# Performance work log

Hardware: AMD Instinct MI355X
Metric: run time of the kernel (lower is better)

Reference implementation:

```python
import jax, jax.numpy as jnp
import numpy as np

C = 512
CTX = 768
HEADS = 8
GROUPS = min(8, C)
EPS = 1e-5


def setup_inputs() -> dict:
    key = jax.random.key(0)
    ks = jax.random.split(key, 10)
    B, H, W, S = 16, 32, 32, 77
    s_in = 1.0 / np.sqrt(C)
    s_ctx = 1.0 / np.sqrt(CTX)
    return {
        "x": jax.random.normal(ks[0], (B, C, H, W), jnp.float32),
        "context": jax.random.normal(ks[1], (B, S, CTX), jnp.float32),
        "gn_w": jnp.ones((C,), jnp.float32),
        "gn_b": jnp.zeros((C,), jnp.float32),
        "q_w": jax.random.normal(ks[2], (C, C), jnp.float32) * s_in,
        "q_b": jnp.zeros((C,), jnp.float32),
        "kv_w": jax.random.normal(ks[3], (2 * C, CTX), jnp.float32) * s_ctx,
        "kv_b": jnp.zeros((2 * C,), jnp.float32),
        "proj_w": jax.random.normal(ks[4], (C, C), jnp.float32) * s_in,
        "proj_b": jnp.zeros((C,), jnp.float32),
    }


def _group_norm(x, w, b):
    # x: [B, C, H, W]; normalize per group over (C/G, H, W)
    B, Cc, H, W = x.shape
    xg = x.reshape(B, GROUPS, Cc // GROUPS, H * W)
    mean = xg.mean(axis=(2, 3), keepdims=True)
    var = xg.var(axis=(2, 3), keepdims=True)
    xn = (xg - mean) * jax.lax.rsqrt(var + EPS)
    xn = xn.reshape(B, Cc, H, W)
    return xn * w[None, :, None, None] + b[None, :, None, None]


def reference(x, context, gn_w, gn_b, q_w, q_b, kv_w, kv_b, proj_w, proj_b):
    B, Cc, H, W = x.shape
    hd = Cc // HEADS
    h = _group_norm(x, gn_w, gn_b).reshape(B, Cc, H * W)
    # 1x1 conv Q == channel-mixing GEMM
    q = jnp.einsum("oc,bcn->bon", q_w, h) + q_b[None, :, None]  # [B, C, HW]
    q = q.reshape(B, HEADS, hd, H * W).transpose(0, 1, 3, 2)      # [B, h, HW, d]
    S = context.shape[1]
    kv = jnp.einsum("bsc,oc->bso", context, kv_w) + kv_b           # [B, S, 2C]
    kv = kv.reshape(B, S, 2, HEADS, hd)
    k = kv[:, :, 0].transpose(0, 2, 1, 3)                          # [B, h, S, d]
    v = kv[:, :, 1].transpose(0, 2, 1, 3)
    scale = hd ** (-0.5)
    attn = jax.nn.softmax(jnp.einsum("bhnd,bhsd->bhns", q, k) * scale, axis=-1)
    out = jnp.einsum("bhns,bhsd->bhnd", attn, v)                   # [B, h, HW, d]
    out = out.transpose(0, 1, 3, 2).reshape(B, Cc, H * W)
    out = jnp.einsum("oc,bcn->bon", proj_w, out) + proj_b[None, :, None]
    return x + out.reshape(B, Cc, H, W)
```

## Files before the change

### kernel.cpp

```cpp
#include <hip/hip_runtime.h>

#define B_   16
#define C_   512
#define HW_  1024
#define S_   77
#define CTX_ 768
#define HEADS_ 8
#define G_   8
#define EPS_ 1e-5f

typedef unsigned short u16;
typedef unsigned int u32;
typedef __attribute__((ext_vector_type(8))) short bfx8;
typedef __attribute__((ext_vector_type(4))) float fx4;

union U2 { u16 h[4]; uint2 v; };

__device__ __forceinline__ u16 f2bf(float f) {
  union { float f; u32 u; } v; v.f = f;
  u32 u = v.u;
  return (u16)((u + 0x7FFFu + ((u >> 16) & 1u)) >> 16);
}

__device__ __forceinline__ void gload16(const u16* g, u16* l) {
  __builtin_amdgcn_global_load_lds((const __attribute__((address_space(1))) u32*)g,
                                   (__attribute__((address_space(3))) u32*)l, 16, 0, 0);
}

__device__ __forceinline__ void castw_body(const float* __restrict__ in,
                                           u16* __restrict__ out, int K, int i, int n4) {
  if (i >= n4) return;
  float4 v = *(const float4*)(in + (size_t)i * 4);
  int K4 = K >> 2;
  int m = i / K4;
  int k = (i - m * K4) * 4;
  int pb = ((k & 63) >> 3) ^ (m & 7);
  size_t dst = (size_t)m * K + (k & ~63) + (pb << 3) + (k & 7);
  U2 pk;
  pk.h[0] = f2bf(v.x); pk.h[1] = f2bf(v.y); pk.h[2] = f2bf(v.z); pk.h[3] = f2bf(v.w);
  *(uint2*)(out + dst) = pk.v;
}

__device__ __forceinline__ void castctx_body(const float* __restrict__ in,
                                             u16* __restrict__ out, int i) {
  if (i >= 16 * 77 * 192) return;
  int rg = i / 192;
  int k = (i - rg * 192) * 4;
  int b = rg / 77, s = rg - b * 77;
  float4 v = *(const float4*)(in + (size_t)i * 4);
  int pb = ((k & 63) >> 3) ^ (s & 7);
  size_t dst = ((size_t)b * 128 + s) * 768 + (k & ~63) + (pb << 3) + (k & 7);
  U2 pk;
  pk.h[0] = f2bf(v.x); pk.h[1] = f2bf(v.y); pk.h[2] = f2bf(v.z); pk.h[3] = f2bf(v.w);
  *(uint2*)(out + dst) = pk.v;
}

__device__ __forceinline__ void gnstats_body(const float* __restrict__ x,
                                             float2* __restrict__ part, int blk, int t) {
  int bg = blk >> 3, slice = blk & 7;
  const float4* x4 = (const float4*)(x + (size_t)bg * 65536);
  float s = 0.f, ss = 0.f;
  #pragma unroll
  for (int j = 0; j < 8; ++j) {
    float4 v = x4[slice * 2048 + j * 256 + t];
    s  += v.x + v.y + v.z + v.w;
    ss += v.x*v.x + v.y*v.y + v.z*v.z + v.w*v.w;
  }
  #pragma unroll
  for (int off = 32; off; off >>= 1) {
    s  += __shfl_down(s, off);
    ss += __shfl_down(ss, off);
  }
  __shared__ float rs[4], rss[4];
  int wid = t >> 6;
  if ((t & 63) == 0) { rs[wid] = s; rss[wid] = ss; }
  __syncthreads();
  if (t == 0)
    part[blk] = make_float2(rs[0] + rs[1] + rs[2] + rs[3],
                            rss[0] + rss[1] + rss[2] + rss[3]);
}

__global__ __launch_bounds__(256) void prep_kernel(const float* __restrict__ q_w,
                                                   const float* __restrict__ kv_w,
                                                   const float* __restrict__ proj_w,
                                                   const float* __restrict__ ctx,
                                                   const float* __restrict__ x,
                                                   u16* __restrict__ qw_bf,
                                                   u16* __restrict__ kvw_bf,
                                                   u16* __restrict__ pjw_bf,
                                                   u16* __restrict__ ctx_bf,
                                                   float2* __restrict__ gpart) {
  int bid = blockIdx.x, t = threadIdx.x;
  if (bid < 256)        castw_body(q_w,    qw_bf,  512, bid * 256 + t, 65536);
  else if (bid < 1024)  castw_body(kv_w,   kvw_bf, 768, (bid - 256) * 256 + t, 196608);
  else if (bid < 1280)  castw_body(proj_w, pjw_bf, 512, (bid - 1024) * 256 + t, 65536);
  else if (bid < 2204)  castctx_body(ctx, ctx_bf, (bid - 1280) * 256 + t);
  else                  gnstats_body(x, gpart, bid - 2204, t);
}

__device__ void gn_apply_body(int blk, const float* __restrict__ x,
                              const float* __restrict__ w,
                              const float* __restrict__ bgn,
                              const float2* __restrict__ gpart,
                              u16* __restrict__ hT, u16* __restrict__ T2) {
  int nt = blk & 7, bg = blk >> 3;
  int batch = bg >> 3, g = bg & 7;
  const float4* x4 = (const float4*)(x + ((size_t)batch * C_ + (size_t)g * 64) * HW_);
  float s = 0.f, ss = 0.f;
  #pragma unroll
  for (int j = 0; j < 8; ++j) { float2 pp = gpart[bg * 8 + j]; s += pp.x; ss += pp.y; }
  const float invN = 1.0f / 65536.0f;
  float mean = s * invN;
  float rstd = rsqrtf(ss * invN - mean * mean + EPS_);
  int t = threadIdx.x;
  int n4i = t & 31;
  int c4b = t >> 5;
  #pragma unroll
  for (int j = 0; j < 2; ++j) {
    int c4 = c4b + j * 8;
    float4 v[4];
    float wcs[4], bcs[4];
    #pragma unroll
    for (int e = 0; e < 4; ++e) {
      int c = c4 * 4 + e;
      v[e] = x4[(size_t)c * 256 + nt * 32 + n4i];
      int cg = g * 64 + c;
      float wc_ = w[cg] * rstd;
      wcs[e] = wc_;
      bcs[e] = bgn[cg] - mean * wc_;
    }
    int cbase = c4 * 4;
    #pragma unroll
    for (int ne = 0; ne < 4; ++ne) {
      int n = n4i * 4 + ne;
      int pb = (cbase >> 3) ^ (n & 7);
      U2 pk;
      pk.h[0] = f2bf(((const float*)&v[0])[ne] * wcs[0] + bcs[0]);
      pk.h[1] = f2bf(((const float*)&v[1])[ne] * wcs[1] + bcs[1]);
      pk.h[2] = f2bf(((const float*)&v[2])[ne] * wcs[2] + bcs[2]);
      pk.h[3] = f2bf(((const float*)&v[3])[ne] * wcs[3] + bcs[3]);
      *(uint2*)&T2[n * 72 + (pb << 3) + (cbase & 7)] = pk.v;
    }
  }
  __syncthreads();
  #pragma unroll
  for (int j = 0; j < 4; ++j) {
    int idx = j * 256 + t;
    int row = idx >> 3, cs = (idx & 7) * 8;
    uint4 vv = *(const uint4*)&T2[row * 72 + cs];
    *(uint4*)(hT + ((size_t)batch * 1024 + nt * 128 + row) * 512 + g * 64 + cs) = vv;
  }
}

__device__ void kvgemm_body(int blk, const u16* __restrict__ A, const u16* __restrict__ Bw,
                            const float* __restrict__ bias,
                            u16* __restrict__ o16a, u16* __restrict__ o16b,
                            u16* __restrict__ SH) {
  u16* As = SH;
  u16* Bs = SH + 4096;
  int t = threadIdx.x;
  int b = blk >> 6;
  int m0 = ((blk >> 5) & 1) * 64;
  int n0 = (blk & 31) * 32;
  const u16* aBase = A + (size_t)b * 98304 + (size_t)(m0 + (t >> 3)) * 768 + (t & 7) * 8;
  const u16* bBase = Bw + (size_t)(n0 + (t >> 3)) * 768 + (t & 7) * 8;
  int wid = t >> 6, l = t & 63;
  int wr = wid & 1, wc = wid >> 1;
  int lr = l & 15, lg = l >> 4, xr = lr & 7;
  fx4 acc[2];
  acc[0] = (fx4){0.f, 0.f, 0.f, 0.f};
  acc[1] = (fx4){0.f, 0.f, 0.f, 0.f};

  for (int k0 = 0; k0 < 768; k0 += 64) {
    __syncthreads();
    #pragma unroll
    for (int i = 0; i < 2; ++i)
      gload16(aBase + k0 + (size_t)i * 32 * 768, As + i * 2048 + t * 8);
    gload16(bBase + k0, Bs + t * 8);
    __syncthreads();
    #pragma unroll
    for (int kk = 0; kk < 2; ++kk) {
      int lb = kk * 4 + lg;
      bfx8 bf = *(const bfx8*)&Bs[(wc * 16 + lr) * 64 + ((lb ^ xr) << 3)];
      #pragma unroll
      for (int mi = 0; mi < 2; ++mi) {
        bfx8 af = *(const bfx8*)&As[(wr * 32 + mi * 16 + lr) * 64 + ((lb ^ xr) << 3)];
        acc[mi] = __builtin_amdgcn_mfma_f32_16x16x32_bf16(af, bf, acc[mi], 0, 0, 0);
      }
    }
  }

  int o = n0 + wc * 16 + lr;
  float bb = bias[o];
  #pragma unroll
  for (int mi = 0; mi < 2; ++mi) {
    int sb = m0 + wr * 32 + mi * 16 + lg * 4;
    if (o < 512) {
      #pragma unroll
      for (int r = 0; r < 4; ++r) {
        int sidx = sb + r;
        if (sidx < 96) {
          int ob = (o & ~63) | (((((o >> 3) & 7) ^ (sidx & 7))) << 3) | (o & 7);
          o16a[(size_t)b * 49152 + (size_t)sidx * 512 + ob] = f2bf(acc[mi][r] + bb);
        }
      }
    } else if (sb < 96) {
      U2 pk;
      #pragma unroll
      for (int r = 0; r < 4; ++r)
        pk.h[r] = (sb + r < S_) ? f2bf(acc[mi][r] + bb) : (u16)0;
      *(uint2*)(o16b + (size_t)b * 49152 + (size_t)(o - 512) * 96 + sb) = pk.v;
    }
  }
}

__global__ __launch_bounds__(256) void mid_kernel(const float* __restrict__ x,
                                                  const float* __restrict__ gn_w,
                                                  const float* __restrict__ gn_b,
                                                  const float2* __restrict__ gpart,
                                                  u16* __restrict__ hT,
                                                  const u16* __restrict__ ctx_bf,
                                                  const u16* __restrict__ kvw_bf,
                                                  const float* __restrict__ kv_b,
                                                  u16* __restrict__ kvT_k,
                                                  u16* __restrict__ kvV) {
  __shared__ u16 SH[9216];
  int bid = blockIdx.x;
  if (bid < 1024) gn_apply_body(bid, x, gn_w, gn_b, gpart, hT, SH);
  else            kvgemm_body(bid - 1024, ctx_bf, kvw_bf, kv_b, kvT_k, kvV, SH);
}

__global__ __launch_bounds__(256) void gemm2_kernel(
    const u16* __restrict__ A, const u16* __restrict__ Bw,
    const float* __restrict__ bias, const float* __restrict__ resid,
    float* __restrict__ outf, int K, size_t strideA)
{
  __shared__ u16 As[128 * 64];
  __shared__ u16 Bs[128 * 64];
  int t = threadIdx.x;
  int b = blockIdx.z;
  int n0 = blockIdx.x * 128, m0 = blockIdx.y * 128;
  const u16* aBase = A + (size_t)b * strideA + (size_t)(m0 + (t >> 3)) * K + (t & 7) * 8;
  const u16* bBase = Bw + (size_t)(n0 + (t >> 3)) * K + (t & 7) * 8;
  int wid = t >> 6, l = t & 63;
  int wr = wid >> 1, wc = wid & 1;
  int lr = l & 15, lg = l >> 4;
  fx4 acc[4][4];
  #pragma unroll
  for (int i = 0; i < 4; ++i)
    #pragma unroll
    for (int j = 0; j < 4; ++j) acc[i][j] = (fx4){0.f, 0.f, 0.f, 0.f};

  for (int k0 = 0; k0 < K; k0 += 64) {
    __syncthreads();
    #pragma unroll
    for (int i = 0; i < 4; ++i) {
      gload16(aBase + k0 + (size_t)i * 32 * K, As + i * 2048 + t * 8);
      gload16(bBase + k0 + (size_t)i * 32 * K, Bs + i * 2048 + t * 8);
    }
    __syncthreads();
    #pragma unroll
    for (int kk = 0; kk < 2; ++kk) {
      bfx8 af[4], bf[4];
      int xr = (lr & 7);
      #pragma unroll
      for (int i = 0; i < 4; ++i) {
        int lb = kk * 4 + lg;
        af[i] = *(const bfx8*)&As[(wr * 64 + i * 16 + lr) * 64 + ((lb ^ xr) << 3)];
        bf[i] = *(const bfx8*)&Bs[(wc * 64 + i * 16 + lr) * 64 + ((lb ^ xr) << 3)];
      }
      #pragma unroll
      for (int mi = 0; mi < 4; ++mi)
        #pragma unroll
        for (int ni = 0; ni < 4; ++ni)
          acc[mi][ni] = __builtin_amdgcn_mfma_f32_16x16x32_bf16(af[mi], bf[ni], acc[mi][ni], 0, 0, 0);
    }
  }

  float* O = outf + (size_t)b * 524288;
  const float* R = resid + (size_t)b * 524288;
  #pragma unroll
  for (int ni = 0; ni < 4; ++ni) {
    int cc = n0 + wc * 64 + ni * 16 + lr;
    float bb = bias[cc];
    #pragma unroll
    for (int mi = 0; mi < 4; ++mi) {
      size_t off = (size_t)cc * 1024 + m0 + wr * 64 + mi * 16 + lg * 4;
      float4 rv = *(const float4*)(R + off);
      float4 ov;
      ov.x = acc[mi][ni][0] + bb + rv.x;
      ov.y = acc[mi][ni][1] + bb + rv.y;
      ov.z = acc[mi][ni][2] + bb + rv.z;
      ov.w = acc[mi][ni][3] + bb + rv.w;
      *(float4*)(O + off) = ov;
    }
  }
}

__global__ __launch_bounds__(256) void qattn_kernel(const u16* __restrict__ hT,
                                                    const u16* __restrict__ qw,
                                                    const float* __restrict__ q_b,
                                                    const u16* __restrict__ kvK,
                                                    const u16* __restrict__ kvV,
                                                    u16* __restrict__ aoT) {
  __shared__ u16 SH[12288];
  u16* QO = SH;
  u16* As = SH + 4096;
  u16* Bs = SH + 8192;
  u16* Ps = SH + 4096;

  int t = threadIdx.x;
  int n0 = blockIdx.x * 64, head = blockIdx.y, b = blockIdx.z;
  int wid = t >> 6, l = t & 63;
  int lr = l & 15, lg = l >> 4, xr = lr & 7;
  int qbase = wid * 16;

  {
    const u16* aBase = hT + (size_t)b * 524288 + (size_t)(n0 + (t >> 3)) * 512 + (t & 7) * 8;
    const u16* bBase = qw + (size_t)(head * 64 + (t >> 3)) * 512 + (t & 7) * 8;
    fx4 acc[4];
    #pragma unroll
    for (int j = 0; j < 4; ++j) acc[j] = (fx4){0.f, 0.f, 0.f, 0.f};
    for (int k0 = 0; k0 < 512; k0 += 64) {
      __syncthreads();
      #pragma unroll
      for (int i = 0; i < 2; ++i) {
        gload16(aBase + k0 + (size_t)i * 32 * 512, As + i * 2048 + t * 8);
        gload16(bBase + k0 + (size_t)i * 32 * 512, Bs + i * 2048 + t * 8);
      }
      __syncthreads();
      #pragma unroll
      for (int kk = 0; kk < 2; ++kk) {
        int lb = kk * 4 + lg;
        bfx8 af = *(const bfx8*)&As[(qbase + lr) * 64 + ((lb ^ xr) << 3)];
        bfx8 bf[4];
        #pragma unroll
        for (int i = 0; i < 4; ++i)
          bf[i] = *(const bfx8*)&Bs[(i * 16 + lr) * 64 + ((lb ^ xr) << 3)];
        #pragma unroll
        for (int ni = 0; ni < 4; ++ni)
          acc[ni] = __builtin_amdgcn_mfma_f32_16x16x32_bf16(af, bf[ni], acc[ni], 0, 0, 0);
      }
    }
    #pragma unroll
    for (int ni = 0; ni < 4; ++ni) {
      int d = ni * 16 + lr;
      float bb = q_b[head * 64 + d];
      #pragma unroll
      for (int r = 0; r < 4; ++r) {
        int q = qbase + lg * 4 + r;
        QO[q * 64 + ((((d >> 3) ^ (q & 7))) << 3) + (d & 7)] = f2bf(acc[ni][r] + bb);
      }
    }
  }
  __syncthreads();

  {
    int row = qbase + (l >> 2), part = l & 3;
    if (part < 2)
      *(uint4*)&Ps[row * 104 + 80 + part * 8] = (uint4){0u, 0u, 0u, 0u};
  }

  const u16* kB = kvK + (size_t)b * 49152 + head * 64;
  {
    int qrow = qbase + lr;
    fx4 sc[5];
    #pragma unroll
    for (int ti = 0; ti < 5; ++ti) sc[ti] = (fx4){0.f, 0.f, 0.f, 0.f};
    #pragma unroll
    for (int ks = 0; ks < 2; ++ks) {
      int kb = ((ks * 4 + lg) ^ xr) << 3;
      bfx8 a = *(const bfx8*)&QO[qrow * 64 + kb];
      #pragma unroll
      for (int ti = 0; ti < 5; ++ti) {
        bfx8 bb = *(const bfx8*)(kB + (size_t)(ti * 16 + lr) * 512 + kb);
        sc[ti] = __builtin_amdgcn_mfma_f32_16x16x32_bf16(a, bb, sc[ti], 0, 0, 0);
      }
    }
    #pragma unroll
    for (int ti = 0; ti < 5; ++ti) {
      bool valid = (ti * 16 + lr) < S_;
      #pragma unroll
      for (int r = 0; r < 4; ++r)
        sc[ti][r] = valid ? sc[ti][r] * 0.125f : -1e30f;
    }
    fx4 mx = sc[0];
    #pragma unroll
    for (int ti = 1; ti < 5; ++ti)
      #pragma unroll
      for (int r = 0; r < 4; ++r) mx[r] = fmaxf(mx[r], sc[ti][r]);
    #pragma unroll
    for (int off = 1; off < 16; off <<= 1)
      #pragma unroll
      for (int r = 0; r < 4; ++r) mx[r] = fmaxf(mx[r], __shfl_xor(mx[r], off));
    fx4 sm = (fx4){0.f, 0.f, 0.f, 0.f};
    #pragma unroll
    for (int ti = 0; ti < 5; ++ti)
      #pragma unroll
      for (int r = 0; r < 4; ++r) {
        float e = __expf(sc[ti][r] - mx[r]);
        sc[ti][r] = e; sm[r] += e;
      }
    #pragma unroll
    for (int off = 1; off < 16; off <<= 1)
      #pragma unroll
      for (int r = 0; r < 4; ++r) sm[r] += __shfl_xor(sm[r], off);
    fx4 inv;
    #pragma unroll
    for (int r = 0; r < 4; ++r) inv[r] = __builtin_amdgcn_rcpf(sm[r]);
    #pragma unroll
    for (int ti = 0; ti < 5; ++ti)
      #pragma unroll
      for (int r = 0; r < 4; ++r)
        Ps[(qbase + lg * 4 + r) * 104 + ti * 16 + lr] = f2bf(sc[ti][r] * inv[r]);
  }

  const u16* vB = kvV + (size_t)b * 49152 + (size_t)head * 64 * 96;
  {
    int q = qbase + lr;
    fx4 o[4];
    #pragma unroll
    for (int dt = 0; dt < 4; ++dt) o[dt] = (fx4){0.f, 0.f, 0.f, 0.f};
    #pragma unroll
    for (int ks = 0; ks < 3; ++ks) {
      bfx8 pb_ = *(const bfx8*)&Ps[q * 104 + ks * 32 + lg * 8];
      #pragma unroll
      for (int dt = 0; dt < 4; ++dt) {
        bfx8 a = *(const bfx8*)(vB + (size_t)(dt * 16 + lr) * 96 + ks * 32 + lg * 8);
        o[dt] = __builtin_amdgcn_mfma_f32_16x16x32_bf16(a, pb_, o[dt], 0, 0, 0);
      }
    }
    #pragma unroll
    for (int dt = 0; dt < 4; ++dt) {
      int db = dt * 16 + lg * 4;
      int pb = ((db >> 3) ^ (q & 7));
      U2 pk;
      #pragma unroll
      for (int r = 0; r < 4; ++r) pk.h[r] = f2bf(o[dt][r]);
      *(uint2*)&QO[q * 64 + (pb << 3) + (db & 7)] = pk.v;
    }
  }
  __syncthreads();

  const size_t aobase = (size_t)b * 524288 + (size_t)n0 * 512 + head * 64;
  #pragma unroll
  for (int j = 0; j < 2; ++j) {
    int idx = j * 256 + t;
    int row = idx >> 3, cs = (idx & 7) * 8;
    *(uint4*)(aoT + aobase + (size_t)row * 512 + cs) = *(const uint4*)&QO[row * 64 + cs];
  }
}

extern "C" void kernel_launch(void* const* d_in, const int* in_sizes, int n_in,
                              void* d_out, int out_size, void* d_ws, size_t ws_size,
                              hipStream_t stream) {
  const float* x      = (const float*)d_in[0];
  const float* ctx    = (const float*)d_in[1];
  const float* gn_w   = (const float*)d_in[2];
  const float* gn_b   = (const float*)d_in[3];
  const float* q_w    = (const float*)d_in[4];
  const float* q_b    = (const float*)d_in[5];
  const float* kv_w   = (const float*)d_in[6];
  const float* kv_b   = (const float*)d_in[7];
  const float* proj_w = (const float*)d_in[8];
  const float* proj_b = (const float*)d_in[9];
  float* out = (float*)d_out;

  u16* p = (u16*)d_ws;
  u16* qw_bf  = p; p += 262144;
  u16* kvw_bf = p; p += 786432;
  u16* pjw_bf = p; p += 262144;
  u16* ctx_bf = p; p += 16 * 128 * 768;
  u16* hT     = p; p += 8388608;
  u16* aoT    = p; p += 8388608;
  u16* kvT_k  = p; p += 16 * 96 * 512;
  u16* kvV    = p; p += 16 * 512 * 96;
  float2* gpart = (float2*)p; p += 1024 * 4;

  prep_kernel<<<3228, 256, 0, stream>>>(q_w, kv_w, proj_w, ctx, x,
                                        qw_bf, kvw_bf, pjw_bf, ctx_bf, gpart);

  mid_kernel<<<2048, 256, 0, stream>>>(x, gn_w, gn_b, gpart, hT,
                                       ctx_bf, kvw_bf, kv_b, kvT_k, kvV);

  qattn_kernel<<<dim3(16, HEADS_, B_), 256, 0, stream>>>(hT, qw_bf, q_b, kvT_k, kvV, aoT);

  gemm2_kernel<<<dim3(4, 8, B_), 256, 0, stream>>>(
      aoT, pjw_bf, proj_b, x, out, 512, (size_t)1024 * 512);
}
```

Measured before the change: 79.53 us.

## Fuse GN stats with raw bf16 transpose; apply affine in place later

The group-norm statistics pass now also transposes x into the bf16 hT buffer unnormalized, so x (32 MB fp32) is read once instead of twice. The mid kernel then reads hT back, applies the per-channel scale and shift from a small shared table, and rewrites it in place. This swaps a second fp32 read of x for a bf16 read-modify-write of hT. It adds a double bf16 rounding, and the prep kernel's larger static shared memory (18 KB for every block) may lower occupancy for the cast blocks.

```diff
diff --git a/kernel.cpp b/kernel.cpp
--- a/kernel.cpp
+++ b/kernel.cpp
@@ -20,6 +20,10 @@
   union { float f; u32 u; } v; v.f = f;
   u32 u = v.u;
   return (u16)((u + 0x7FFFu + ((u >> 16) & 1u)) >> 16);
+}
+__device__ __forceinline__ float bf2f(u16 h) {
+  union { u32 u; float f; } v; v.u = ((u32)h) << 16;
+  return v.f;
 }
 
 __device__ __forceinline__ void gload16(const u16* g, u16* l) {
@@ -55,29 +59,57 @@
   *(uint2*)(out + dst) = pk.v;
 }
 
-__device__ __forceinline__ void gnstats_body(const float* __restrict__ x,
-                                             float2* __restrict__ part, int blk, int t) {
-  int bg = blk >> 3, slice = blk & 7;
-  const float4* x4 = (const float4*)(x + (size_t)bg * 65536);
+__device__ void gntrans_body(int blk, const float* __restrict__ x,
+                             u16* __restrict__ hT, float2* __restrict__ part,
+                             u16* __restrict__ T2, float* rs, float* rss) {
+  int t = threadIdx.x;
+  int nt = blk & 7, bg = blk >> 3;
+  int batch = bg >> 3, g = bg & 7;
+  const float4* x4 = (const float4*)(x + ((size_t)batch * C_ + (size_t)g * 64) * HW_);
+  int n4i = t & 31;
+  int c4b = t >> 5;
   float s = 0.f, ss = 0.f;
   #pragma unroll
-  for (int j = 0; j < 8; ++j) {
-    float4 v = x4[slice * 2048 + j * 256 + t];
-    s  += v.x + v.y + v.z + v.w;
-    ss += v.x*v.x + v.y*v.y + v.z*v.z + v.w*v.w;
+  for (int j = 0; j < 2; ++j) {
+    int c4 = c4b + j * 8;
+    float4 v[4];
+    #pragma unroll
+    for (int e = 0; e < 4; ++e) {
+      v[e] = x4[(size_t)(c4 * 4 + e) * 256 + nt * 32 + n4i];
+      s  += v[e].x + v[e].y + v[e].z + v[e].w;
+      ss += v[e].x*v[e].x + v[e].y*v[e].y + v[e].z*v[e].z + v[e].w*v[e].w;
+    }
+    int cbase = c4 * 4;
+    #pragma unroll
+    for (int ne = 0; ne < 4; ++ne) {
+      int n = n4i * 4 + ne;
+      int pb = (cbase >> 3) ^ (n & 7);
+      U2 pk;
+      pk.h[0] = f2bf(((const float*)&v[0])[ne]);
+      pk.h[1] = f2bf(((const float*)&v[1])[ne]);
+      pk.h[2] = f2bf(((const float*)&v[2])[ne]);
+      pk.h[3] = f2bf(((const float*)&v[3])[ne]);
+      *(uint2*)&T2[n * 72 + (pb << 3) + (cbase & 7)] = pk.v;
+    }
   }
   #pragma unroll
   for (int off = 32; off; off >>= 1) {
     s  += __shfl_down(s, off);
     ss += __shfl_down(ss, off);
   }
-  __shared__ float rs[4], rss[4];
   int wid = t >> 6;
   if ((t & 63) == 0) { rs[wid] = s; rss[wid] = ss; }
   __syncthreads();
   if (t == 0)
     part[blk] = make_float2(rs[0] + rs[1] + rs[2] + rs[3],
                             rss[0] + rss[1] + rss[2] + rss[3]);
+  #pragma unroll
+  for (int j = 0; j < 4; ++j) {
+    int idx = j * 256 + t;
+    int row = idx >> 3, cs = (idx & 7) * 8;
+    uint4 vv = *(const uint4*)&T2[row * 72 + cs];
+    *(uint4*)(hT + ((size_t)batch * 1024 + nt * 128 + row) * 512 + g * 64 + cs) = vv;
+  }
 }
 
 __global__ __launch_bounds__(256) void prep_kernel(const float* __restrict__ q_w,
@@ -89,66 +121,55 @@
                                                    u16* __restrict__ kvw_bf,
                                                    u16* __restrict__ pjw_bf,
                                                    u16* __restrict__ ctx_bf,
+                                                   u16* __restrict__ hT,
                                                    float2* __restrict__ gpart) {
+  __shared__ u16 T2[9216];
+  __shared__ float rs[4], rss[4];
   int bid = blockIdx.x, t = threadIdx.x;
   if (bid < 256)        castw_body(q_w,    qw_bf,  512, bid * 256 + t, 65536);
   else if (bid < 1024)  castw_body(kv_w,   kvw_bf, 768, (bid - 256) * 256 + t, 196608);
   else if (bid < 1280)  castw_body(proj_w, pjw_bf, 512, (bid - 1024) * 256 + t, 65536);
   else if (bid < 2204)  castctx_body(ctx, ctx_bf, (bid - 1280) * 256 + t);
-  else                  gnstats_body(x, gpart, bid - 2204, t);
-}
-
-__device__ void gn_apply_body(int blk, const float* __restrict__ x,
-                              const float* __restrict__ w,
-                              const float* __restrict__ bgn,
-                              const float2* __restrict__ gpart,
-                              u16* __restrict__ hT, u16* __restrict__ T2) {
+  else                  gntrans_body(bid - 2204, x, hT, gpart, T2, rs, rss);
+}
+
+__device__ void gnaff_body(int blk, const float* __restrict__ w,
+                           const float* __restrict__ bgn,
+                           const float2* __restrict__ gpart,
+                           u16* __restrict__ hT, float* tab) {
+  int t = threadIdx.x;
   int nt = blk & 7, bg = blk >> 3;
   int batch = bg >> 3, g = bg & 7;
-  const float4* x4 = (const float4*)(x + ((size_t)batch * C_ + (size_t)g * 64) * HW_);
   float s = 0.f, ss = 0.f;
   #pragma unroll
   for (int j = 0; j < 8; ++j) { float2 pp = gpart[bg * 8 + j]; s += pp.x; ss += pp.y; }
   const float invN = 1.0f / 65536.0f;
   float mean = s * invN;
   float rstd = rsqrtf(ss * invN - mean * mean + EPS_);
-  int t = threadIdx.x;
-  int n4i = t & 31;
-  int c4b = t >> 5;
-  #pragma unroll
-  for (int j = 0; j < 2; ++j) {
-    int c4 = c4b + j * 8;
-    float4 v[4];
-    float wcs[4], bcs[4];
-    #pragma unroll
-    for (int e = 0; e < 4; ++e) {
-      int c = c4 * 4 + e;
-      v[e] = x4[(size_t)c * 256 + nt * 32 + n4i];
-      int cg = g * 64 + c;
-      float wc_ = w[cg] * rstd;
-      wcs[e] = wc_;
-      bcs[e] = bgn[cg] - mean * wc_;
-    }
-    int cbase = c4 * 4;
-    #pragma unroll
-    for (int ne = 0; ne < 4; ++ne) {
-      int n = n4i * 4 + ne;
-      int pb = (cbase >> 3) ^ (n & 7);
-      U2 pk;
-      pk.h[0] = f2bf(((const float*)&v[0])[ne] * wcs[0] + bcs[0]);
-      pk.h[1] = f2bf(((const float*)&v[1])[ne] * wcs[1] + bcs[1]);
-      pk.h[2] = f2bf(((const float*)&v[2])[ne] * wcs[2] + bcs[2]);
-      pk.h[3] = f2bf(((const float*)&v[3])[ne] * wcs[3] + bcs[3]);
-      *(uint2*)&T2[n * 72 + (pb << 3) + (cbase & 7)] = pk.v;
-    }
+  if (t < 64) {
+    float wc = w[g * 64 + t] * rstd;
+    tab[t] = wc;
+    tab[64 + t] = bgn[g * 64 + t] - mean * wc;
   }
   __syncthreads();
+  u16* base = hT + ((size_t)batch * 1024 + (size_t)nt * 128) * 512 + g * 64;
   #pragma unroll
   for (int j = 0; j < 4; ++j) {
     int idx = j * 256 + t;
-    int row = idx >> 3, cs = (idx & 7) * 8;
-    uint4 vv = *(const uint4*)&T2[row * 72 + cs];
-    *(uint4*)(hT + ((size_t)batch * 1024 + nt * 128 + row) * 512 + g * 64 + cs) = vv;
+    int row = idx >> 3, jb = idx & 7;
+    u16* pp = base + (size_t)row * 512 + jb * 8;
+    uint4 v = *(const uint4*)pp;
+    const u16* hv = (const u16*)&v;
+    int ch = (jb ^ (row & 7)) << 3;
+    U2 lo, hi;
+    #pragma unroll
+    for (int e = 0; e < 4; ++e)
+      lo.h[e] = f2bf(bf2f(hv[e]) * tab[ch + e] + tab[64 + ch + e]);
+    #pragma unroll
+    for (int e = 0; e < 4; ++e)
+      hi.h[e] = f2bf(bf2f(hv[4 + e]) * tab[ch + 4 + e] + tab[64 + ch + 4 + e]);
+    uint4 o; o.x = lo.v.x; o.y = lo.v.y; o.z = hi.v.x; o.w = hi.v.y;
+    *(uint4*)pp = o;
   }
 }
 
@@ -214,8 +235,7 @@
   }
 }
 
-__global__ __launch_bounds__(256) void mid_kernel(const float* __restrict__ x,
-                                                  const float* __restrict__ gn_w,
+__global__ __launch_bounds__(256) void mid_kernel(const float* __restrict__ gn_w,
                                                   const float* __restrict__ gn_b,
                                                   const float2* __restrict__ gpart,
                                                   u16* __restrict__ hT,
@@ -224,9 +244,9 @@
                                                   const float* __restrict__ kv_b,
                                                   u16* __restrict__ kvT_k,
                                                   u16* __restrict__ kvV) {
-  __shared__ u16 SH[9216];
+  __shared__ u16 SH[6144];
   int bid = blockIdx.x;
-  if (bid < 1024) gn_apply_body(bid, x, gn_w, gn_b, gpart, hT, SH);
+  if (bid < 1024) gnaff_body(bid, gn_w, gn_b, gpart, hT, (float*)SH);
   else            kvgemm_body(bid - 1024, ctx_bf, kvw_bf, kv_b, kvT_k, kvV, SH);
 }
 
@@ -478,9 +498,9 @@
   float2* gpart = (float2*)p; p += 1024 * 4;
 
   prep_kernel<<<3228, 256, 0, stream>>>(q_w, kv_w, proj_w, ctx, x,
-                                        qw_bf, kvw_bf, pjw_bf, ctx_bf, gpart);
-
-  mid_kernel<<<2048, 256, 0, stream>>>(x, gn_w, gn_b, gpart, hT,
+                                        qw_bf, kvw_bf, pjw_bf, ctx_bf, hT, gpart);
+
+  mid_kernel<<<2048, 256, 0, stream>>>(gn_w, gn_b, gpart, hT,
                                        ctx_bf, kvw_bf, kv_b, kvT_k, kvV);
 
   qattn_kernel<<<dim3(16, HEADS_, B_), 256, 0, stream>>>(hT, qw_bf, q_b, kvT_k, kvV, aoT);
```

Result: slower. 81.47 us (+2.4%).
